# Optimization experiments

Hardware: AMD Instinct MI355X
Metric: run time of the kernel (lower is better)

## Reference

```python
import jax, jax.numpy as jnp
import numpy as np

N = 8192        # nodes
IN_F = 256      # in_features
OUT_F = 64      # out_features per head
HEADS = 4
ALPHA = 0.2     # leaky relu slope
NEG_INF = -9e15


def setup_inputs() -> dict:
    key = jax.random.key(0)
    ks = jax.random.split(key, 8)
    h = jax.random.normal(ks[0], (N, IN_F), dtype=jnp.float32)
    adj = jax.random.randint(ks[1], (N, N), 0, 2, dtype=jnp.int32)
    # per-head GAT params, stacked over heads
    W = jax.random.normal(ks[2], (HEADS, IN_F, OUT_F), dtype=jnp.float32) * (1.0 / np.sqrt(IN_F))
    a1 = jax.random.normal(ks[3], (HEADS, OUT_F), dtype=jnp.float32) * (1.0 / np.sqrt(OUT_F))
    a2 = jax.random.normal(ks[4], (HEADS, OUT_F), dtype=jnp.float32) * (1.0 / np.sqrt(OUT_F))
    # fusing linear: Linear(out*heads, out)
    fc_w = jax.random.normal(ks[5], (OUT_F, HEADS * OUT_F), dtype=jnp.float32) * (1.0 / np.sqrt(HEADS * OUT_F))
    fc_b = jax.random.normal(ks[6], (OUT_F,), dtype=jnp.float32) * 0.01
    return {"h": h, "adj": adj, "W": W, "a1": a1, "a2": a2, "fc_w": fc_w, "fc_b": fc_b}


def reference(h, adj, W, a1, a2, fc_w, fc_b):
    # all heads batched: Wh [H, N, F]
    Wh = jnp.einsum('ni,hio->hno', h, W)
    # attention logits e_ij = leakyrelu(a1.Wh_i + a2.Wh_j), shape [H, N, N]
    e_src = jnp.einsum('hno,ho->hn', Wh, a1)   # [H, N]
    e_dst = jnp.einsum('hno,ho->hn', Wh, a2)   # [H, N]
    e = jax.nn.leaky_relu(e_src[:, :, None] + e_dst[:, None, :], ALPHA)
    e = jnp.where(adj[None] > 0, e, NEG_INF)
    attn = jax.nn.softmax(e, axis=-1)          # masked softmax over neighbors
    out = jnp.einsum('hnm,hmo->hno', attn, Wh)  # [H, N, F]
    out = jax.nn.elu(out)
    # concat heads along feature dim -> [N, H*F], then fuse linear
    h_concat = jnp.transpose(out, (1, 0, 2)).reshape(N, HEADS * OUT_F)
    return h_concat @ fc_w.T + fc_b
```

## Files before the change

### kernel.cpp

```cpp
#include <hip/hip_runtime.h>
#include <hip/hip_bf16.h>

#define NN 8192
#define NHEADS 4
#define NCHUNK 4
#define CHUNK 2048
#define LOG2E 1.4426950408889634f

typedef __bf16 bf16x8 __attribute__((ext_vector_type(8)));
typedef float fx4 __attribute__((ext_vector_type(4)));
typedef int ix4 __attribute__((ext_vector_type(4)));
typedef unsigned short ushort8 __attribute__((ext_vector_type(8)));

__device__ __forceinline__ float bf2f(unsigned short u) {
  return __builtin_bit_cast(float, ((unsigned)u) << 16);
}

__global__ __launch_bounds__(256) void k_wh(
    const float* __restrict__ h, const float* __restrict__ W,
    const float* __restrict__ a1, const float* __restrict__ a2,
    const float* __restrict__ fcw, unsigned short* __restrict__ whsw,
    float* __restrict__ R, float* __restrict__ F1, float* __restrict__ F2,
    float* __restrict__ fcwT)
{
  __shared__ float ws[64 * 260];
  const int tid = threadIdx.x;
  const int bx = blockIdx.x;

  if (bx == 512) {
    for (int idx = tid; idx < 64 * 256; idx += 256) {
      int o = idx >> 8, c = idx & 255;
      fcwT[c * 64 + o] = fcw[o * 256 + c];
    }
    return;
  }

  const int hd = bx >> 7;
  const int i0 = (bx & 127) << 6;

  const float* Wp = W + hd * (256 * 64);
  for (int idx = tid; idx < 256 * 64; idx += 256) {
    int k = idx >> 6, o = idx & 63;
    ws[o * 260 + k] = Wp[idx];
  }
  __syncthreads();

  const int w = tid >> 6, o = tid & 63;
  const int ibase = i0 + w * 16;
  float acc[16];
#pragma unroll
  for (int m = 0; m < 16; ++m) acc[m] = 0.f;

  const float* hp = h + (size_t)ibase * 256;
  for (int k4 = 0; k4 < 64; ++k4) {
    fx4 wv = *(const fx4*)(&ws[o * 260 + k4 * 4]);
#pragma unroll
    for (int m = 0; m < 16; ++m) {
      fx4 hv = *(const fx4*)(hp + m * 256 + k4 * 4);
      acc[m] += hv[0] * wv[0] + hv[1] * wv[1] + hv[2] * wv[2] + hv[3] * wv[3];
    }
  }

  const float a1v = a1[hd * 64 + o], a2v = a2[hd * 64 + o];
#pragma unroll
  for (int m = 0; m < 16; ++m) {
    float s1 = acc[m] * a1v, s2 = acc[m] * a2v;
#pragma unroll
    for (int d = 1; d < 64; d <<= 1) {
      s1 += __shfl_xor(s1, d);
      s2 += __shfl_xor(s2, d);
    }
    if (o == 0) {
      int ix = hd * NN + ibase + m;
      R[ix]  = __builtin_amdgcn_exp2f(-0.8f * s1 * LOG2E);
      F1[ix] = __builtin_amdgcn_exp2f(s2 * LOG2E);
      F2[ix] = __builtin_amdgcn_exp2f(0.2f * s2 * LOG2E);
    }
  }

  size_t base = (size_t)hd * 524288 + (size_t)((i0 >> 5) + (w >> 1)) * 2048 +
                (size_t)(o >> 4) * 512;
  int ln0 = (o & 15) + 16 * ((w & 1) * 2);
  ushort8 pk0, pk1;
#pragma unroll
  for (int m = 0; m < 8; ++m) {
    pk0[m] = __builtin_bit_cast(unsigned short, (__bf16)acc[m]);
    pk1[m] = __builtin_bit_cast(unsigned short, (__bf16)acc[m + 8]);
  }
  *(ushort8*)(whsw + base + (size_t)ln0 * 8) = pk0;
  *(ushort8*)(whsw + base + (size_t)(ln0 + 16) * 8) = pk1;
}

struct Tile {
  fx4 f1a, f1b, f2a, f2b;
  bf16x8 b0, b1, b2, b3;
  unsigned m0, m1;
};

__device__ __forceinline__ void load_tile(Tile& t, const float* F1p,
                                          const float* F2p,
                                          const unsigned short* wp,
                                          const unsigned* bml, int il, int jb)
{
  t.f1a = *(const fx4*)(F1p + jb);
  t.f1b = *(const fx4*)(F1p + jb + 4);
  t.f2a = *(const fx4*)(F2p + jb);
  t.f2b = *(const fx4*)(F2p + jb + 4);
  const unsigned short* wq = wp + (size_t)(jb >> 5) * 2048;
  t.b0 = *(const bf16x8*)(wq);
  t.b1 = *(const bf16x8*)(wq + 512);
  t.b2 = *(const bf16x8*)(wq + 1024);
  t.b3 = *(const bf16x8*)(wq + 1536);
  const unsigned* mb = bml + (jb >> 5) * 33;
  t.m0 = mb[il];
  t.m1 = mb[16 + il];
}

__device__ __forceinline__ void compute_tile(const Tile& t, const float* Rr,
                                             int g, const bf16x8& ones,
                                             fx4 acc[2][4], fx4* accS)
{
#pragma unroll
  for (int rs = 0; rs < 2; ++rs) {
    unsigned sm = (rs ? t.m1 : t.m0) >> (g * 8);
    float p[8];
#pragma unroll
    for (int e = 0; e < 8; ++e) {
      float f1 = (e < 4) ? t.f1a[e] : t.f1b[e - 4];
      float f2 = (e < 4) ? t.f2a[e] : t.f2b[e - 4];
      float pm = fmaxf(f1, Rr[rs] * f2);
      unsigned keep = (unsigned)(((int)(sm << (31 - e))) >> 31);
      p[e] = __builtin_bit_cast(float,
                 __builtin_bit_cast(unsigned, pm) & keep);
    }
    bf16x8 af;
#pragma unroll
    for (int e = 0; e < 8; ++e) af[e] = (__bf16)p[e];
    acc[rs][0] = __builtin_amdgcn_mfma_f32_16x16x32_bf16(af, t.b0, acc[rs][0], 0, 0, 0);
    acc[rs][1] = __builtin_amdgcn_mfma_f32_16x16x32_bf16(af, t.b1, acc[rs][1], 0, 0, 0);
    acc[rs][2] = __builtin_amdgcn_mfma_f32_16x16x32_bf16(af, t.b2, acc[rs][2], 0, 0, 0);
    acc[rs][3] = __builtin_amdgcn_mfma_f32_16x16x32_bf16(af, t.b3, acc[rs][3], 0, 0, 0);
    accS[rs] = __builtin_amdgcn_mfma_f32_16x16x32_bf16(af, ones, accS[rs], 0, 0, 0);
  }
}

__global__ __launch_bounds__(256) void k_attn(
    const int* __restrict__ adj, const unsigned short* __restrict__ whsw,
    const float* __restrict__ Rg, const float* __restrict__ F1g,
    const float* __restrict__ F2g, unsigned short* __restrict__ paccB,
    float* __restrict__ psum)
{
  __shared__ unsigned bml[(CHUNK / 32) * 33];
  const int tid = threadIdx.x;
  const int lane = tid & 63;
  const int hd = tid >> 6;
  const int bx = blockIdx.x;
  const int xcd = bx & 7;
  const int ci = xcd >> 1;
  const int rt = ((bx >> 3) << 1) | (xcd & 1);
  const int i0 = rt << 5;
  const int j0 = ci * CHUNK;
  const int il = lane & 15;
  const int g = lane >> 4;

  {
    const int* ap = adj + (size_t)(i0 + hd * 8) * NN + j0 + lane * 32;
    ix4 vA[8], vB[8];
#pragma unroll
    for (int u = 0; u < 8; ++u)
      vA[u] = *(const ix4*)(ap + u * 4);

#pragma unroll
    for (int i = 0; i < 8; ++i) {
      ix4* cur = (i & 1) ? vB : vA;
      ix4* nxt = (i & 1) ? vA : vB;
      if (i < 7) {
        const int* np = ap + (size_t)(i + 1) * NN;
#pragma unroll
        for (int u = 0; u < 8; ++u)
          nxt[u] = *(const ix4*)(np + u * 4);
      }
      unsigned wrd = 0;
#pragma unroll
      for (int u = 0; u < 8; ++u) {
        wrd |= ((unsigned)cur[u][0]) << (u * 4 + 0);
        wrd |= ((unsigned)cur[u][1]) << (u * 4 + 1);
        wrd |= ((unsigned)cur[u][2]) << (u * 4 + 2);
        wrd |= ((unsigned)cur[u][3]) << (u * 4 + 3);
      }
      bml[lane * 33 + hd * 8 + i] = wrd;
    }
  }
  __syncthreads();

  float Rr[2];
#pragma unroll
  for (int rs = 0; rs < 2; ++rs)
    Rr[rs] = Rg[hd * NN + i0 + rs * 16 + il];
  const float* F1p = F1g + hd * NN + j0 + g * 8;
  const float* F2p = F2g + hd * NN + j0 + g * 8;
  const unsigned short* wp = whsw + (size_t)hd * 524288 +
                             (size_t)(j0 >> 5) * 2048 + (size_t)lane * 8;
  bf16x8 ones;
#pragma unroll
  for (int e = 0; e < 8; ++e) ones[e] = (__bf16)1.0f;

  fx4 acc[2][4] = {};
  fx4 accS[2] = {};

  Tile t0, t1;
  load_tile(t0, F1p, F2p, wp, bml, il, 0);
  for (int jb = 0; jb < CHUNK; jb += 64) {
    load_tile(t1, F1p, F2p, wp, bml, il, jb + 32);
    compute_tile(t0, Rr, g, ones, acc, accS);
    if (jb + 64 < CHUNK) load_tile(t0, F1p, F2p, wp, bml, il, jb + 64);
    compute_tile(t1, Rr, g, ones, acc, accS);
  }

#pragma unroll
  for (int rs = 0; rs < 2; ++rs) {
    if (il == 0) {
#pragma unroll
      for (int r = 0; r < 4; ++r)
        psum[(size_t)(ci * NHEADS + hd) * NN + i0 + rs * 16 + g * 4 + r] =
            accS[rs][r];
    }
  }

  unsigned short* pc = paccB + (size_t)ci * NN * 256;
#pragma unroll
  for (int rs = 0; rs < 2; ++rs)
#pragma unroll
    for (int r = 0; r < 4; ++r)
#pragma unroll
      for (int ft = 0; ft < 4; ++ft)
        pc[(size_t)(i0 + rs * 16 + g * 4 + r) * 256 + hd * 64 + ft * 16 + il] =
            __builtin_bit_cast(unsigned short, (__bf16)acc[rs][ft][r]);
}

__global__ __launch_bounds__(256) void k_fc(
    const unsigned short* __restrict__ paccB, const float* __restrict__ psum,
    const float* __restrict__ fcwT, const float* __restrict__ fcb,
    float* __restrict__ out)
{
  __shared__ float ash[32 * 260];
  __shared__ float inv[32 * 4];
  const int tid = threadIdx.x;
  const int i0 = blockIdx.x * 32;

  if (tid < 128) {
    int m = tid >> 2, hh = tid & 3;
    float s = 0.f;
#pragma unroll
    for (int ci = 0; ci < NCHUNK; ++ci)
      s += psum[(size_t)(ci * NHEADS + hh) * NN + i0 + m];
    inv[m * 4 + hh] = 1.0f / s;
  }
  __syncthreads();

  for (int idx = tid; idx < 32 * 32; idx += 256) {
    int m = idx & 31, c8 = idx >> 5;
    size_t off = ((size_t)(i0 + m)) * 256 + c8 * 8;
    float v[8] = {0.f, 0.f, 0.f, 0.f, 0.f, 0.f, 0.f, 0.f};
#pragma unroll
    for (int ci = 0; ci < NCHUNK; ++ci) {
      ushort8 a = *(const ushort8*)(paccB + (size_t)ci * NN * 256 + off);
#pragma unroll
      for (int j = 0; j < 8; ++j) v[j] += bf2f(a[j]);
    }
    float iv = inv[m * 4 + (c8 >> 3)];
#pragma unroll
    for (int j = 0; j < 8; ++j) {
      float x = v[j] * iv;
      x = (x > 0.f) ? x : (__builtin_amdgcn_exp2f(x * LOG2E) - 1.0f);
      ash[m * 260 + c8 * 8 + j] = x;
    }
  }
  __syncthreads();

  const int w = tid >> 6, o = tid & 63;
  float acc[8];
#pragma unroll
  for (int m = 0; m < 8; ++m) acc[m] = 0.f;

  for (int c4 = 0; c4 < 64; ++c4) {
    float w0 = fcwT[(c4 * 4 + 0) * 64 + o];
    float w1 = fcwT[(c4 * 4 + 1) * 64 + o];
    float w2 = fcwT[(c4 * 4 + 2) * 64 + o];
    float w3 = fcwT[(c4 * 4 + 3) * 64 + o];
#pragma unroll
    for (int m = 0; m < 8; ++m) {
      fx4 hv = *(const fx4*)(&ash[(w * 8 + m) * 260 + c4 * 4]);
      acc[m] += hv[0] * w0 + hv[1] * w1 + hv[2] * w2 + hv[3] * w3;
    }
  }
  const float bo = fcb[o];
#pragma unroll
  for (int m = 0; m < 8; ++m)
    out[(size_t)(i0 + w * 8 + m) * 64 + o] = acc[m] + bo;
}

extern "C" void kernel_launch(void* const* d_in, const int* in_sizes, int n_in,
                              void* d_out, int out_size, void* d_ws, size_t ws_size,
                              hipStream_t stream) {
  (void)in_sizes; (void)n_in; (void)out_size; (void)ws_size;
  const float* h   = (const float*)d_in[0];
  const int*   adj = (const int*)d_in[1];
  const float* W   = (const float*)d_in[2];
  const float* a1  = (const float*)d_in[3];
  const float* a2  = (const float*)d_in[4];
  const float* fcw = (const float*)d_in[5];
  const float* fcb = (const float*)d_in[6];
  float* out = (float*)d_out;

  char* base = (char*)d_ws;
  unsigned short* whsw = (unsigned short*)base;
  float* R  = (float*)(base + (4u << 20));
  float* F1 = (float*)(base + (4u << 20) + (128u << 10));
  float* F2 = (float*)(base + (4u << 20) + (256u << 10));
  float* psum = (float*)(base + (5u << 20));
  float* fcwT = (float*)(base + (6u << 20));
  unsigned short* paccB = (unsigned short*)(base + (7u << 20));

  k_wh<<<dim3(513), dim3(256), 0, stream>>>(h, W, a1, a2, fcw, whsw, R, F1, F2, fcwT);
  k_attn<<<dim3(1024), dim3(256), 0, stream>>>(adj, whsw, R, F1, F2, paccB, psum);
  k_fc<<<dim3(256), dim3(256), 0, stream>>>(paccB, psum, fcwT, fcb, out);
}
```

Measured before the change: 248.9 us.

## Fuse final linear into attention kernel via last-block atomic counter

Removes the separate k_fc launch. Each attention block increments a per-row-tile counter, and the last of the four chunk blocks for a tile performs the normalization, ELU and fused linear. A memset of the counters is added before the kernels. This increases k_attn shared memory usage, which may lower occupancy, and adds fence/atomic overhead.

```diff
diff --git a/kernel.cpp b/kernel.cpp
--- a/kernel.cpp
+++ b/kernel.cpp
@@ -148,9 +148,14 @@
     const int* __restrict__ adj, const unsigned short* __restrict__ whsw,
     const float* __restrict__ Rg, const float* __restrict__ F1g,
     const float* __restrict__ F2g, unsigned short* __restrict__ paccB,
-    float* __restrict__ psum)
+    float* __restrict__ psum, unsigned* __restrict__ cnt,
+    const float* __restrict__ fcwT, const float* __restrict__ fcb,
+    float* __restrict__ out)
 {
   __shared__ unsigned bml[(CHUNK / 32) * 33];
+  __shared__ float ash[32 * 260];
+  __shared__ float inv[32 * 4];
+  __shared__ int is_last;
   const int tid = threadIdx.x;
   const int lane = tid & 63;
   const int hd = tid >> 6;
@@ -236,24 +241,21 @@
       for (int ft = 0; ft < 4; ++ft)
         pc[(size_t)(i0 + rs * 16 + g * 4 + r) * 256 + hd * 64 + ft * 16 + il] =
             __builtin_bit_cast(unsigned short, (__bf16)acc[rs][ft][r]);
-}
-
-__global__ __launch_bounds__(256) void k_fc(
-    const unsigned short* __restrict__ paccB, const float* __restrict__ psum,
-    const float* __restrict__ fcwT, const float* __restrict__ fcb,
-    float* __restrict__ out)
-{
-  __shared__ float ash[32 * 260];
-  __shared__ float inv[32 * 4];
-  const int tid = threadIdx.x;
-  const int i0 = blockIdx.x * 32;
+
+  __threadfence();
+  __syncthreads();
+  if (tid == 0)
+    is_last = (atomicAdd(&cnt[rt], 1u) == NCHUNK - 1);
+  __syncthreads();
+  if (!is_last) return;
+  __threadfence();
 
   if (tid < 128) {
     int m = tid >> 2, hh = tid & 3;
     float s = 0.f;
 #pragma unroll
-    for (int ci = 0; ci < NCHUNK; ++ci)
-      s += psum[(size_t)(ci * NHEADS + hh) * NN + i0 + m];
+    for (int c = 0; c < NCHUNK; ++c)
+      s += psum[(size_t)(c * NHEADS + hh) * NN + i0 + m];
     inv[m * 4 + hh] = 1.0f / s;
   }
   __syncthreads();
@@ -263,8 +265,8 @@
     size_t off = ((size_t)(i0 + m)) * 256 + c8 * 8;
     float v[8] = {0.f, 0.f, 0.f, 0.f, 0.f, 0.f, 0.f, 0.f};
 #pragma unroll
-    for (int ci = 0; ci < NCHUNK; ++ci) {
-      ushort8 a = *(const ushort8*)(paccB + (size_t)ci * NN * 256 + off);
+    for (int c = 0; c < NCHUNK; ++c) {
+      ushort8 a = *(const ushort8*)(paccB + (size_t)c * NN * 256 + off);
 #pragma unroll
       for (int j = 0; j < 8; ++j) v[j] += bf2f(a[j]);
     }
@@ -279,9 +281,9 @@
   __syncthreads();
 
   const int w = tid >> 6, o = tid & 63;
-  float acc[8];
-#pragma unroll
-  for (int m = 0; m < 8; ++m) acc[m] = 0.f;
+  float facc[8];
+#pragma unroll
+  for (int m = 0; m < 8; ++m) facc[m] = 0.f;
 
   for (int c4 = 0; c4 < 64; ++c4) {
     float w0 = fcwT[(c4 * 4 + 0) * 64 + o];
@@ -291,13 +293,13 @@
 #pragma unroll
     for (int m = 0; m < 8; ++m) {
       fx4 hv = *(const fx4*)(&ash[(w * 8 + m) * 260 + c4 * 4]);
-      acc[m] += hv[0] * w0 + hv[1] * w1 + hv[2] * w2 + hv[3] * w3;
+      facc[m] += hv[0] * w0 + hv[1] * w1 + hv[2] * w2 + hv[3] * w3;
     }
   }
   const float bo = fcb[o];
 #pragma unroll
   for (int m = 0; m < 8; ++m)
-    out[(size_t)(i0 + w * 8 + m) * 64 + o] = acc[m] + bo;
+    out[(size_t)(i0 + w * 8 + m) * 64 + o] = facc[m] + bo;
 }
 
 extern "C" void kernel_launch(void* const* d_in, const int* in_sizes, int n_in,
@@ -320,9 +322,11 @@
   float* F2 = (float*)(base + (4u << 20) + (256u << 10));
   float* psum = (float*)(base + (5u << 20));
   float* fcwT = (float*)(base + (6u << 20));
+  unsigned* cnt = (unsigned*)(base + (6u << 20) + (64u << 10));
   unsigned short* paccB = (unsigned short*)(base + (7u << 20));
 
+  hipMemsetAsync(cnt, 0, 256 * sizeof(unsigned), stream);
   k_wh<<<dim3(513), dim3(256), 0, stream>>>(h, W, a1, a2, fcw, whsw, R, F1, F2, fcwT);
-  k_attn<<<dim3(1024), dim3(256), 0, stream>>>(adj, whsw, R, F1, F2, paccB, psum);
-  k_fc<<<dim3(256), dim3(256), 0, stream>>>(paccB, psum, fcwT, fcb, out);
-}
+  k_attn<<<dim3(1024), dim3(256), 0, stream>>>(adj, whsw, R, F1, F2, paccB,
+                                               psum, cnt, fcwT, fcb, out);
+}
```

Result: slower. 444.4 us (+78.6%).

## Move adjacency bitmask packing into the prep kernel alongside Wh projection

Applied to the files above, without the earlier changes.

Packing the int32 adjacency matrix into bitmasks now happens in 2048 extra blocks of the first kernel, which run concurrently with the Wh projection blocks. The attention kernel then loads precomputed 32-bit mask words from a workspace buffer instead of streaming 256 MB of adjacency itself. The Wh projection also drops its shared-memory staging of W and reads W directly from global/cache with strided loads. This adds a global bitmask write and read round trip and changes the W access pattern, which may be less efficient.

```diff
diff --git a/kernel.cpp b/kernel.cpp
--- a/kernel.cpp
+++ b/kernel.cpp
@@ -5,6 +5,7 @@
 #define NHEADS 4
 #define NCHUNK 4
 #define CHUNK 2048
+#define NWH 512
 #define LOG2E 1.4426950408889634f
 
 typedef __bf16 bf16x8 __attribute__((ext_vector_type(8)));
@@ -16,18 +17,19 @@
   return __builtin_bit_cast(float, ((unsigned)u) << 16);
 }
 
-__global__ __launch_bounds__(256) void k_wh(
+__global__ __launch_bounds__(256) void k_prep(
+    const int* __restrict__ adj, unsigned* __restrict__ bm,
     const float* __restrict__ h, const float* __restrict__ W,
     const float* __restrict__ a1, const float* __restrict__ a2,
     const float* __restrict__ fcw, unsigned short* __restrict__ whsw,
     float* __restrict__ R, float* __restrict__ F1, float* __restrict__ F2,
     float* __restrict__ fcwT)
 {
-  __shared__ float ws[64 * 260];
   const int tid = threadIdx.x;
   const int bx = blockIdx.x;
-
-  if (bx == 512) {
+  const int lane = tid & 63;
+
+  if (bx == NWH + 2048) {
     for (int idx = tid; idx < 64 * 256; idx += 256) {
       int o = idx >> 8, c = idx & 255;
       fcwT[c * 64 + o] = fcw[o * 256 + c];
@@ -35,29 +37,57 @@
     return;
   }
 
+  if (bx >= NWH) {
+    const int row = (bx - NWH) * 4 + (tid >> 6);
+    const int* ap = adj + (size_t)row * NN + lane * 32;
+    unsigned* bp = bm + (size_t)row * 256 + lane;
+
+    ix4 vA[8], vB[8];
+#pragma unroll
+    for (int u = 0; u < 8; ++u) vA[u] = *(const ix4*)(ap + u * 4);
+
+#pragma unroll
+    for (int it = 0; it < 4; ++it) {
+      ix4* cur = (it & 1) ? vB : vA;
+      ix4* nxt = (it & 1) ? vA : vB;
+      if (it < 3) {
+#pragma unroll
+        for (int u = 0; u < 8; ++u)
+          nxt[u] = *(const ix4*)(ap + (it + 1) * 2048 + u * 4);
+      }
+      unsigned wrd = 0;
+#pragma unroll
+      for (int u = 0; u < 8; ++u) {
+        wrd |= ((unsigned)cur[u][0]) << (u * 4 + 0);
+        wrd |= ((unsigned)cur[u][1]) << (u * 4 + 1);
+        wrd |= ((unsigned)cur[u][2]) << (u * 4 + 2);
+        wrd |= ((unsigned)cur[u][3]) << (u * 4 + 3);
+      }
+      bp[it * 64] = wrd;
+    }
+    return;
+  }
+
   const int hd = bx >> 7;
   const int i0 = (bx & 127) << 6;
-
-  const float* Wp = W + hd * (256 * 64);
-  for (int idx = tid; idx < 256 * 64; idx += 256) {
-    int k = idx >> 6, o = idx & 63;
-    ws[o * 260 + k] = Wp[idx];
-  }
-  __syncthreads();
-
   const int w = tid >> 6, o = tid & 63;
   const int ibase = i0 + w * 16;
+
   float acc[16];
 #pragma unroll
   for (int m = 0; m < 16; ++m) acc[m] = 0.f;
 
   const float* hp = h + (size_t)ibase * 256;
+  const float* Wp = W + hd * (256 * 64) + o;
   for (int k4 = 0; k4 < 64; ++k4) {
-    fx4 wv = *(const fx4*)(&ws[o * 260 + k4 * 4]);
+    float w0 = Wp[(k4 * 4 + 0) * 64];
+    float w1 = Wp[(k4 * 4 + 1) * 64];
+    float w2 = Wp[(k4 * 4 + 2) * 64];
+    float w3 = Wp[(k4 * 4 + 3) * 64];
 #pragma unroll
     for (int m = 0; m < 16; ++m) {
       fx4 hv = *(const fx4*)(hp + m * 256 + k4 * 4);
-      acc[m] += hv[0] * wv[0] + hv[1] * wv[1] + hv[2] * wv[2] + hv[3] * wv[3];
+      acc[m] += hv[0] * w0 + hv[1] * w1 + hv[2] * w2 + hv[3] * w3;
     }
   }
 
@@ -145,7 +175,7 @@
 }
 
 __global__ __launch_bounds__(256) void k_attn(
-    const int* __restrict__ adj, const unsigned short* __restrict__ whsw,
+    const unsigned* __restrict__ bm, const unsigned short* __restrict__ whsw,
     const float* __restrict__ Rg, const float* __restrict__ F1g,
     const float* __restrict__ F2g, unsigned short* __restrict__ paccB,
     float* __restrict__ psum)
@@ -163,33 +193,11 @@
   const int il = lane & 15;
   const int g = lane >> 4;
 
-  {
-    const int* ap = adj + (size_t)(i0 + hd * 8) * NN + j0 + lane * 32;
-    ix4 vA[8], vB[8];
-#pragma unroll
-    for (int u = 0; u < 8; ++u)
-      vA[u] = *(const ix4*)(ap + u * 4);
-
-#pragma unroll
-    for (int i = 0; i < 8; ++i) {
-      ix4* cur = (i & 1) ? vB : vA;
-      ix4* nxt = (i & 1) ? vA : vB;
-      if (i < 7) {
-        const int* np = ap + (size_t)(i + 1) * NN;
-#pragma unroll
-        for (int u = 0; u < 8; ++u)
-          nxt[u] = *(const ix4*)(np + u * 4);
-      }
-      unsigned wrd = 0;
-#pragma unroll
-      for (int u = 0; u < 8; ++u) {
-        wrd |= ((unsigned)cur[u][0]) << (u * 4 + 0);
-        wrd |= ((unsigned)cur[u][1]) << (u * 4 + 1);
-        wrd |= ((unsigned)cur[u][2]) << (u * 4 + 2);
-        wrd |= ((unsigned)cur[u][3]) << (u * 4 + 3);
-      }
-      bml[lane * 33 + hd * 8 + i] = wrd;
-    }
+  for (int it = 0; it < 8; ++it) {
+    int idx = it * 256 + tid;
+    int r = idx >> 6, w = idx & 63;
+    unsigned v = bm[(size_t)(i0 + r) * 256 + (j0 >> 5) + w];
+    bml[w * 33 + r] = v;
   }
   __syncthreads();
 
@@ -320,9 +328,12 @@
   float* F2 = (float*)(base + (4u << 20) + (256u << 10));
   float* psum = (float*)(base + (5u << 20));
   float* fcwT = (float*)(base + (6u << 20));
-  unsigned short* paccB = (unsigned short*)(base + (7u << 20));
-
-  k_wh<<<dim3(513), dim3(256), 0, stream>>>(h, W, a1, a2, fcw, whsw, R, F1, F2, fcwT);
-  k_attn<<<dim3(1024), dim3(256), 0, stream>>>(adj, whsw, R, F1, F2, paccB, psum);
+  unsigned* bmask = (unsigned*)(base + (8u << 20));
+  unsigned short* paccB = (unsigned short*)(base + (16u << 20));
+
+  k_prep<<<dim3(NWH + 2048 + 1), dim3(256), 0, stream>>>(
+      adj, bmask, h, W, a1, a2, fcw, whsw, R, F1, F2, fcwT);
+  k_attn<<<dim3(1024), dim3(256), 0, stream>>>(bmask, whsw, R, F1, F2,
+                                               paccB, psum);
   k_fc<<<dim3(256), dim3(256), 0, stream>>>(paccB, psum, fcwT, fcb, out);
 }
```

Result: no change. 252.1 us (+1.3%).
